# Optimization experiments

Measured on AMD Instinct MI355X. Metric: run time of the kernel, lower is better.

## Reference

```python
import jax, jax.numpy as jnp
import numpy as np

HIDDEN = 2048
N_HEADS = 32
N_KV_HEADS = 8
HEAD_DIM = HIDDEN // N_HEADS  # 64
ROPE_BASE = 10000.0
B, S = 2, 2048
NEG_INF = -1e9


def rotate_half(x):
    x1, x2 = jnp.split(x, 2, axis=-1)
    return jnp.concatenate((-x2, x1), axis=-1)


def rope_cos_sin(seq_len, head_dim, base, dtype):
    inv_freq = 1.0 / (base ** (jnp.arange(0, head_dim, 2, dtype=jnp.float32) / head_dim))
    pos = jnp.arange(seq_len, dtype=jnp.float32)
    freqs = jnp.outer(pos, inv_freq)              # [S, D/2]
    emb = jnp.concatenate((freqs, freqs), axis=-1)  # [S, D]
    return jnp.cos(emb).astype(dtype)[None, None], jnp.sin(emb).astype(dtype)[None, None]


def setup_inputs() -> dict:
    key = jax.random.key(0)
    ks = jax.random.split(key, 5)
    hidden_states = jax.random.normal(ks[0], (B, S, HIDDEN), dtype=jnp.float32)
    # causal additive mask, Llama-style
    causal = jnp.tril(jnp.ones((S, S), dtype=bool))
    attention_mask = jnp.where(causal, 0.0, NEG_INF).astype(jnp.float32)
    attention_mask = jnp.broadcast_to(attention_mask[None, None], (B, 1, S, S))
    sc = 1.0 / np.sqrt(HIDDEN)
    Wq = jax.random.normal(ks[1], (HIDDEN, HIDDEN), dtype=jnp.float32) * sc
    Wk = jax.random.normal(ks[2], (N_KV_HEADS * HEAD_DIM, HIDDEN), dtype=jnp.float32) * sc
    Wv = jax.random.normal(ks[3], (N_KV_HEADS * HEAD_DIM, HIDDEN), dtype=jnp.float32) * sc
    Wo = jax.random.normal(ks[4], (HIDDEN, HIDDEN), dtype=jnp.float32) * sc
    return {"hidden_states": hidden_states, "attention_mask": attention_mask,
            "Wq": Wq, "Wk": Wk, "Wv": Wv, "Wo": Wo}


def reference(hidden_states, attention_mask, Wq, Wk, Wv, Wo):
    b, s, _ = hidden_states.shape
    groups = N_HEADS // N_KV_HEADS
    # projections (torch Linear: x @ W.T)
    q = (hidden_states @ Wq.T).reshape(b, s, N_HEADS, HEAD_DIM).transpose(0, 2, 1, 3)      # [b,H,s,d]
    k = (hidden_states @ Wk.T).reshape(b, s, N_KV_HEADS, HEAD_DIM).transpose(0, 2, 1, 3)   # [b,Hk,s,d]
    v = (hidden_states @ Wv.T).reshape(b, s, N_KV_HEADS, HEAD_DIM).transpose(0, 2, 1, 3)
    cos, sin = rope_cos_sin(s, HEAD_DIM, ROPE_BASE, hidden_states.dtype)
    q = q * cos + rotate_half(q) * sin
    k = k * cos + rotate_half(k) * sin
    # GQA without materializing repeated K/V: view q as [b, Hk, g, s, d]
    qg = q.reshape(b, N_KV_HEADS, groups, s, HEAD_DIM)
    scores = jnp.einsum('bhgqd,bhkd->bhgqk', qg, k) / np.sqrt(HEAD_DIM)  # [b,Hk,g,s,s]
    scores = scores + attention_mask[:, :, None]                          # mask [b,1,1,s,s]
    probs = jax.nn.softmax(scores.astype(jnp.float32), axis=-1).astype(q.dtype)
    attn = jnp.einsum('bhgqk,bhkd->bhgqd', probs, v)                      # [b,Hk,g,s,d]
    attn = attn.reshape(b, N_HEADS, s, HEAD_DIM).transpose(0, 2, 1, 3).reshape(b, s, HIDDEN)
    return attn @ Wo.T
```

## Files before the change

kernel.cpp:

```cpp
#include <hip/hip_runtime.h>
#include <math.h>

#define HID 2048
#define NH 32
#define NKV 8
#define HD 64
#define BB 2
#define SS 2048
#define MTOT (BB * SS)

typedef __bf16 bf16;
typedef __bf16 bf16x8 __attribute__((ext_vector_type(8)));
typedef __bf16 bf16x4 __attribute__((ext_vector_type(4)));
typedef float f32x4 __attribute__((ext_vector_type(4)));

#define MFMA16(a, b, c) __builtin_amdgcn_mfma_f32_16x16x32_bf16((a), (b), (c), 0, 0, 0)

__device__ __forceinline__ void load_lds16(const void* g, void* l) {
  __builtin_amdgcn_global_load_lds((const __attribute__((address_space(1))) void*)g,
                                   (__attribute__((address_space(3))) void*)l, 16, 0, 0);
}

#define FENCE() asm volatile("" ::: "memory")
#define SYNC_VM(N) do { FENCE(); \
  asm volatile("s_waitcnt vmcnt(" #N ") lgkmcnt(0)" ::: "memory"); \
  __builtin_amdgcn_s_barrier(); FENCE(); } while (0)

__global__ void cvt_all(const float* __restrict__ hs, const float* __restrict__ Wq,
                        const float* __restrict__ Wk, const float* __restrict__ Wv,
                        const float* __restrict__ Wo,
                        bf16* __restrict__ A_b, bf16* __restrict__ Wq_b,
                        bf16* __restrict__ Wk_b, bf16* __restrict__ Wv_b,
                        bf16* __restrict__ Wo_b) {
  int bid = blockIdx.x;
  const float* src;
  bf16* dst;
  if (bid < 8192)       { src = hs; dst = A_b; }
  else if (bid < 12288) { src = Wq; dst = Wq_b; bid -= 8192; }
  else if (bid < 13312) { src = Wk; dst = Wk_b; bid -= 12288; }
  else if (bid < 14336) { src = Wv; dst = Wv_b; bid -= 13312; }
  else                  { src = Wo; dst = Wo_b; bid -= 14336; }
  int i = (bid * 256 + threadIdx.x) * 4;
  float4 v = *(const float4*)(src + i);
  bf16x4 o;
  o[0] = (bf16)v.x; o[1] = (bf16)v.y; o[2] = (bf16)v.z; o[3] = (bf16)v.w;
  *(bf16x4*)(dst + i) = o;
}

__device__ __forceinline__ void gemm_core_k64(const char* Agc, const char* Bgc,
                                              char* lds, f32x4 (&acc)[4][4]) {
  constexpr int ABYTES = 32768;
  constexpr int BUFB = 49152;
  constexpr int NT = HID / 64;

  const int tid = threadIdx.x;
  const int w = tid >> 6, lane = tid & 63;
  const int l16 = lane & 15, quad = lane >> 4;
  const int wr = w >> 1, wc = w & 1;
  const int wb = w * 1024;

  const int cu = (lane & 7) ^ ((lane >> 3) & 7);
  const char* gA = Agc + (size_t)(w * 8 + (lane >> 3)) * 4096 + cu * 16;
  const char* gB = Bgc + (size_t)(w * 8 + (lane >> 3)) * 4096 + cu * 16;

  const int aswz = l16 & 7;
  const int a_k0 = ((0 + quad) ^ aswz) * 16;
  const int a_k1 = ((4 + quad) ^ aswz) * 16;
  const int arow = (wr * 64 + l16) * 128;
  const int brow = (wc * 64 + l16) * 128;

#pragma unroll
  for (int t0 = 0; t0 < 2; ++t0) {
    char* lb = lds + t0 * BUFB;
#pragma unroll
    for (int j = 0; j < 4; ++j)
      load_lds16(gA + (size_t)j * (64 * 4096) + t0 * 128, lb + wb + j * 8192);
#pragma unroll
    for (int j = 0; j < 2; ++j)
      load_lds16(gB + (size_t)j * (64 * 4096) + t0 * 128, lb + ABYTES + wb + j * 8192);
  }

  char* cur = lds;
  char* stg = lds + 2 * BUFB;
  for (int kt = 0; kt < NT; ++kt) {
    SYNC_VM(6);
    const int ks = (kt + 2 < NT) ? (kt + 2) : (NT - 1);
    const size_t ko = (size_t)ks * 128;

#pragma unroll
    for (int j = 0; j < 4; ++j)
      load_lds16(gA + (size_t)j * (64 * 4096) + ko, stg + wb + j * 8192);
#pragma unroll
    for (int j = 0; j < 2; ++j)
      load_lds16(gB + (size_t)j * (64 * 4096) + ko, stg + ABYTES + wb + j * 8192);
    FENCE();

    const char* Ac = cur;
    const char* Bc = cur + ABYTES;
    bf16x8 af0[4], af1[4], bf0[4], bf1[4];
#pragma unroll
    for (int ni = 0; ni < 4; ++ni) {
      bf0[ni] = *(const bf16x8*)(Bc + brow + ni * 2048 + a_k0);
      bf1[ni] = *(const bf16x8*)(Bc + brow + ni * 2048 + a_k1);
    }
#pragma unroll
    for (int mi = 0; mi < 4; ++mi) {
      af0[mi] = *(const bf16x8*)(Ac + arow + mi * 2048 + a_k0);
      af1[mi] = *(const bf16x8*)(Ac + arow + mi * 2048 + a_k1);
    }
    __builtin_amdgcn_s_setprio(1);
#pragma unroll
    for (int mi = 0; mi < 4; ++mi)
#pragma unroll
      for (int ni = 0; ni < 4; ++ni) {
        acc[mi][ni] = MFMA16(af0[mi], bf0[ni], acc[mi][ni]);
        acc[mi][ni] = MFMA16(af1[mi], bf1[ni], acc[mi][ni]);
      }
    __builtin_amdgcn_s_setprio(0);

    cur = (cur == lds + 2 * BUFB) ? lds : cur + BUFB;
    stg = (stg == lds + 2 * BUFB) ? lds : stg + BUFB;
  }
  asm volatile("s_waitcnt vmcnt(0)" ::: "memory");
}

#define QSCALE 0.1803368801f
#define L2B 0.4152410118f
__global__ __launch_bounds__(512, 2) void gemm_qkv(const bf16* __restrict__ A,
                                                   const bf16* __restrict__ Wq,
                                                   const bf16* __restrict__ Wk,
                                                   const bf16* __restrict__ Wv,
                                                   bf16* __restrict__ Qb,
                                                   bf16* __restrict__ Kb,
                                                   bf16* __restrict__ Vt) {
  __shared__ __align__(16) char lds[3 * 49152];
  const int tileM = blockIdx.x * 256;
  const int n0 = blockIdx.y * 128;
  const bf16* Wp;
  int mode;
  if (n0 < HID) { Wp = Wq + (size_t)n0 * HID; mode = 0; }
  else if (n0 < HID + 512) { Wp = Wk + (size_t)(n0 - HID) * HID; mode = 1; }
  else { Wp = Wv + (size_t)(n0 - HID - 512) * HID; mode = 2; }

  f32x4 acc[4][4];
#pragma unroll
  for (int i = 0; i < 4; ++i)
#pragma unroll
    for (int j = 0; j < 4; ++j) acc[i][j] = (f32x4){0.f, 0.f, 0.f, 0.f};

  gemm_core_k64((const char*)(A + (size_t)tileM * HID), (const char*)Wp, lds, acc);

  const int tid = threadIdx.x;
  const int w = tid >> 6, lane = tid & 63;
  const int l16 = lane & 15, quad = lane >> 4;
  const int wr = w >> 1, wc = w & 1;
  const int mbase = tileM + wr * 64;
  const int cb = n0 + wc * 64;

  if (mode == 2) {
#pragma unroll
    for (int mi = 0; mi < 4; ++mi)
#pragma unroll
      for (int ni = 0; ni < 4; ++ni)
#pragma unroll
        for (int r = 0; r < 4; ++r) {
          int grow = mbase + mi * 16 + quad * 4 + r;
          int b = grow >> 11, spos = grow & (SS - 1);
          int nv = cb + ni * 16 + l16 - (HID + 512);
          Vt[(((size_t)(b * NKV + (nv >> 6))) * HD + (nv & 63)) * SS + spos] =
              (bf16)acc[mi][ni][r];
        }
  } else {
    const float inv0 = __builtin_amdgcn_exp2f(-(float)l16 * L2B);
    const float inv1 = __builtin_amdgcn_exp2f(-(float)(l16 + 16) * L2B);
#pragma unroll
    for (int mi = 0; mi < 4; ++mi) {
#pragma unroll
      for (int r = 0; r < 4; ++r) {
        int grow = mbase + mi * 16 + quad * 4 + r;
        int b = grow >> 11, spos = grow & (SS - 1);
        float sn0, cs0, sn1, cs1;
        sincosf((float)spos * inv0, &sn0, &cs0);
        sincosf((float)spos * inv1, &sn1, &cs1);
        float a0 = acc[mi][0][r], a1 = acc[mi][1][r];
        float a2 = acc[mi][2][r], a3 = acc[mi][3][r];
        float o0 = a0 * cs0 - a2 * sn0;
        float o2 = a2 * cs0 + a0 * sn0;
        float o1 = a1 * cs1 - a3 * sn1;
        float o3 = a3 * cs1 + a1 * sn1;
        if (mode == 0) {
          bf16* qp = Qb + (size_t)grow * HID + cb + l16;
          qp[0]  = (bf16)(o0 * QSCALE);
          qp[16] = (bf16)(o1 * QSCALE);
          qp[32] = (bf16)(o2 * QSCALE);
          qp[48] = (bf16)(o3 * QSCALE);
        } else {
          int kvh = (cb - HID) >> 6;
          bf16* kp = Kb + ((size_t)(b * NKV + kvh) * SS + spos) * HD + l16;
          kp[0]  = (bf16)o0;
          kp[16] = (bf16)o1;
          kp[32] = (bf16)o2;
          kp[48] = (bf16)o3;
        }
      }
    }
  }
}

__global__ __launch_bounds__(512, 2) void gemm_out(const bf16* __restrict__ A,
                                                   const bf16* __restrict__ Wo,
                                                   float* __restrict__ out) {
  __shared__ __align__(16) char lds[3 * 49152];
  const int tileM = blockIdx.x * 256;
  const int n0 = blockIdx.y * 128;
  f32x4 acc[4][4];
#pragma unroll
  for (int i = 0; i < 4; ++i)
#pragma unroll
    for (int j = 0; j < 4; ++j) acc[i][j] = (f32x4){0.f, 0.f, 0.f, 0.f};

  gemm_core_k64((const char*)(A + (size_t)tileM * HID),
                (const char*)(Wo + (size_t)n0 * HID), lds, acc);

  const int tid = threadIdx.x;
  const int w = tid >> 6, lane = tid & 63;
  const int l16 = lane & 15, quad = lane >> 4;
  const int wr = w >> 1, wc = w & 1;
#pragma unroll
  for (int mi = 0; mi < 4; ++mi)
#pragma unroll
    for (int ni = 0; ni < 4; ++ni)
#pragma unroll
      for (int r = 0; r < 4; ++r) {
        int grow = tileM + wr * 64 + mi * 16 + quad * 4 + r;
        int gcol = n0 + wc * 64 + ni * 16 + l16;
        out[(size_t)grow * HID + gcol] = acc[mi][ni][r];
      }
}

#define PSTR 72
__global__ __launch_bounds__(256, 3) void attn(const bf16* __restrict__ Qb,
                                               const bf16* __restrict__ Kb,
                                               const bf16* __restrict__ Vt,
                                               bf16* __restrict__ Ctx) {
  __shared__ bf16 Ktile[2][64 * 64];
  __shared__ bf16 Vtile[2][64 * 64];
  __shared__ bf16 Pbuf[4][32 * PSTR];
  const int tid = threadIdx.x;
  const int w = tid >> 6, lane = tid & 63;
  const int l16 = lane & 15, quad = lane >> 4;
  const int bh = blockIdx.y, b = bh >> 5, h = bh & 31, kvh = h >> 2;
  bf16* Pw = &Pbuf[w][0];
  const char* Kslice = (const char*)(Kb + ((size_t)(b * NKV + kvh)) * SS * HD);
  const char* Vslice = (const char*)(Vt + ((size_t)(b * NKV + kvh)) * HD * SS);
  const int qrel = w * 16 + l16;

  const int srow = (lane >> 3) & 7;
  const int pchunk = ((lane & 7) ^ srow) << 4;
  const int so = ((quad ^ (l16 & 7)) << 4);
  const int so2 = so ^ 64;

  const int xA = (int)blockIdx.x;

  int cur = 0;
  {
#pragma unroll
    for (int i = 0; i < 2; ++i) {
      const int r = w * 16 + i * 8 + srow;
      load_lds16(Kslice + (size_t)r * 128 + pchunk,
                 (char*)Ktile[0] + (w * 16 + i * 8) * 128);
      load_lds16(Vslice + (size_t)r * 4096 + pchunk,
                 (char*)Vtile[0] + (w * 16 + i * 8) * 128);
    }
  }

  for (int t = 0; t < 2; ++t) {
    const int X = t ? (15 - xA) : xA;
    const int qA = X * 128 + qrel;
    const int ktmax = 2 * X + 1;

    const bf16* QpA = Qb + ((size_t)(b * SS + qA)) * HID + h * HD + quad * 8;
    bf16x8 qa0 = *(const bf16x8*)QpA;
    bf16x8 qa1 = *(const bf16x8*)(QpA + 32);
    const bf16* QpB = QpA + (size_t)64 * HID;
    bf16x8 qbB0 = *(const bf16x8*)QpB;
    bf16x8 qbB1 = *(const bf16x8*)(QpB + 32);

    float lA = 0.f, lB = 0.f;
    f32x4 oA[4], oB[4];
#pragma unroll
    for (int d = 0; d < 4; ++d) {
      oA[d] = (f32x4){0.f, 0.f, 0.f, 0.f};
      oB[d] = (f32x4){0.f, 0.f, 0.f, 0.f};
    }

    for (int kt = 0; kt <= ktmax; ++kt) {
      __syncthreads();

      const bool have_next = (kt < ktmax) || (t == 0);
      if (have_next) {
        const int nkb = (kt < ktmax) ? (kt + 1) * 64 : 0;
        const int nb = cur ^ 1;
#pragma unroll
        for (int i = 0; i < 2; ++i) {
          const int r = w * 16 + i * 8 + srow;
          load_lds16(Kslice + (size_t)(nkb + r) * 128 + pchunk,
                     (char*)Ktile[nb] + (w * 16 + i * 8) * 128);
          load_lds16(Vslice + (size_t)r * 4096 + (size_t)nkb * 2 + pchunk,
                     (char*)Vtile[nb] + (w * 16 + i * 8) * 128);
        }
      }

      const char* Kc = (const char*)Ktile[cur] + l16 * 128;
      const char* Vc = (const char*)Vtile[cur] + l16 * 128;
      const bool skipA = (kt == ktmax);
      const bool diagA = (kt == ktmax - 1);
      const bool diagB = (kt == ktmax);

#pragma unroll
      for (int nt = 0; nt < 4; ++nt) {
        bf16x8 kf0 = *(const bf16x8*)(Kc + nt * 2048 + so);
        bf16x8 kf1 = *(const bf16x8*)(Kc + nt * 2048 + so2);
        const int krel = nt * 16 + quad * 4;

        bf16x4 pkA;
        if (skipA) {
          pkA[0] = (bf16)0.f; pkA[1] = (bf16)0.f;
          pkA[2] = (bf16)0.f; pkA[3] = (bf16)0.f;
        } else {
          f32x4 s = {0.f, 0.f, 0.f, 0.f};
          s = MFMA16(kf0, qa0, s);
          s = MFMA16(kf1, qa1, s);
          if (diagA) {
#pragma unroll
            for (int r = 0; r < 4; ++r) {
              float p = (krel + r > qrel) ? 0.f : __builtin_amdgcn_exp2f(s[r]);
              lA += p;
              pkA[r] = (bf16)p;
            }
          } else {
#pragma unroll
            for (int r = 0; r < 4; ++r) {
              float p = __builtin_amdgcn_exp2f(s[r]);
              lA += p;
              pkA[r] = (bf16)p;
            }
          }
        }
        *(bf16x4*)&Pw[l16 * PSTR + krel] = pkA;

        f32x4 sB = {0.f, 0.f, 0.f, 0.f};
        sB = MFMA16(kf0, qbB0, sB);
        sB = MFMA16(kf1, qbB1, sB);
        bf16x4 pkB;
        if (diagB) {
#pragma unroll
          for (int r = 0; r < 4; ++r) {
            float p = (krel + r > qrel) ? 0.f : __builtin_amdgcn_exp2f(sB[r]);
            lB += p;
            pkB[r] = (bf16)p;
          }
        } else {
#pragma unroll
          for (int r = 0; r < 4; ++r) {
            float p = __builtin_amdgcn_exp2f(sB[r]);
            lB += p;
            pkB[r] = (bf16)p;
          }
        }
        *(bf16x4*)&Pw[(16 + l16) * PSTR + krel] = pkB;
      }

      bf16x8 pA0 = *(const bf16x8*)&Pw[l16 * PSTR + quad * 8];
      bf16x8 pA1 = *(const bf16x8*)&Pw[l16 * PSTR + 32 + quad * 8];
      bf16x8 pB0 = *(const bf16x8*)&Pw[(16 + l16) * PSTR + quad * 8];
      bf16x8 pB1 = *(const bf16x8*)&Pw[(16 + l16) * PSTR + 32 + quad * 8];
#pragma unroll
      for (int dn = 0; dn < 4; ++dn) {
        bf16x8 v0 = *(const bf16x8*)(Vc + dn * 2048 + so);
        bf16x8 v1 = *(const bf16x8*)(Vc + dn * 2048 + so2);
        oA[dn] = MFMA16(v0, pA0, oA[dn]);
        oA[dn] = MFMA16(v1, pA1, oA[dn]);
        oB[dn] = MFMA16(v0, pB0, oB[dn]);
        oB[dn] = MFMA16(v1, pB1, oB[dn]);
      }
      cur ^= 1;
    }

    lA += __shfl_xor(lA, 16);
    lA += __shfl_xor(lA, 32);
    lB += __shfl_xor(lB, 16);
    lB += __shfl_xor(lB, 32);
    const float invA = 1.0f / lA;
    const float invB = 1.0f / lB;
    bf16* CpA = Ctx + ((size_t)(b * SS + qA)) * HID + h * HD + quad * 4;
    bf16* CpB = CpA + (size_t)64 * HID;
#pragma unroll
    for (int dn = 0; dn < 4; ++dn) {
      bf16x4 ovA, ovB;
#pragma unroll
      for (int r = 0; r < 4; ++r) {
        ovA[r] = (bf16)(oA[dn][r] * invA);
        ovB[r] = (bf16)(oB[dn][r] * invB);
      }
      *(bf16x4*)(CpA + dn * 16) = ovA;
      *(bf16x4*)(CpB + dn * 16) = ovB;
    }
  }
}

extern "C" void kernel_launch(void* const* d_in, const int* in_sizes, int n_in,
                              void* d_out, int out_size, void* d_ws, size_t ws_size,
                              hipStream_t stream) {
  const float* hs = (const float*)d_in[0];
  const float* Wq = (const float*)d_in[2];
  const float* Wk = (const float*)d_in[3];
  const float* Wv = (const float*)d_in[4];
  const float* Wo = (const float*)d_in[5];

  char* ws = (char*)d_ws;
  bf16* A_b  = (bf16*)(ws);
  bf16* Wq_b = (bf16*)(ws + 16777216);
  bf16* Wk_b = (bf16*)(ws + 25165824);
  bf16* Wv_b = (bf16*)(ws + 27262976);
  bf16* Wo_b = (bf16*)(ws + 29360128);
  bf16* Qb   = (bf16*)(ws + 37748736);
  bf16* Kb   = (bf16*)(ws + 54525952);
  bf16* Vt   = (bf16*)(ws + 58720256);
  bf16* Ctx  = A_b;

  cvt_all<<<18432, 256, 0, stream>>>(hs, Wq, Wk, Wv, Wo, A_b, Wq_b, Wk_b, Wv_b, Wo_b);
  gemm_qkv<<<dim3(MTOT / 256, 24), 512, 0, stream>>>(A_b, Wq_b, Wk_b, Wv_b, Qb, Kb, Vt);
  attn<<<dim3(8, BB * NH), 256, 0, stream>>>(Qb, Kb, Vt, Ctx);
  gemm_out<<<dim3(MTOT / 256, HID / 128), 512, 0, stream>>>(Ctx, Wo_b, (float*)d_out);
}
```

Baseline: 296.7 us.

## Use K=32 triple-buffered GEMM core for QKV and split out-proj loads into halves

The QKV projection switches to a new GEMM core with K-step 32, half the LDS footprint (3x24KB) and a new swizzled layout, and its launch bounds are raised to 4 blocks per CU. The goal is more resident blocks to hide memory latency. The output projection keeps K=64 but splits each step into two halves with an extra barrier, so the B-tile prefetch is issued after the first half of the MFMAs. The cost is more loop iterations and barriers per K, plus possible register pressure at the higher occupancy target.

```diff
diff --git a/kernel.cpp b/kernel.cpp
--- a/kernel.cpp
+++ b/kernel.cpp
@@ -47,8 +47,70 @@
   *(bf16x4*)(dst + i) = o;
 }
 
-__device__ __forceinline__ void gemm_core_k64(const char* Agc, const char* Bgc,
-                                              char* lds, f32x4 (&acc)[4][4]) {
+__device__ __forceinline__ void gemm_core256x128(const char* Agc, const char* Bgc,
+                                                 char* lds, f32x4 (&acc)[4][4]) {
+  constexpr int ABYTES = 16384;
+  constexpr int BUFB = 24576;
+  constexpr int NT = HID / 32;
+
+  const int tid = threadIdx.x;
+  const int w = tid >> 6, lane = tid & 63;
+  const int l16 = lane & 15, quad = lane >> 4;
+  const int wr = w >> 1, wc = w & 1;
+  const int wb = w * 1024;
+
+  const int cu = (tid & 7) ^ ((tid >> 3) & 7);
+  const int srcR0 = 2 * (tid >> 3) + (cu >> 2);
+  const int srcC = (cu & 3) * 16;
+  const char* gA = Agc + (size_t)srcR0 * (HID * 2) + srcC;
+  const char* gB = Bgc + (size_t)srcR0 * (HID * 2) + srcC;
+
+  const int acg16 = ((((l16 & 1) << 2) | quad) ^ ((l16 >> 1) & 7)) * 16;
+  const int aoff = (wr * 32 + (l16 >> 1)) * 128 + acg16;
+  const int boff = ABYTES + (wc * 32 + (l16 >> 1)) * 128 + acg16;
+
+#pragma unroll
+  for (int t0 = 0; t0 < 2; ++t0) {
+    char* lb = lds + t0 * BUFB;
+    load_lds16(gA + t0 * 64, lb + wb);
+    load_lds16(gA + (size_t)128 * (HID * 2) + t0 * 64, lb + 8192 + wb);
+    load_lds16(gB + t0 * 64, lb + ABYTES + wb);
+  }
+
+  char* cur = lds;
+  char* stg = lds + 2 * BUFB;
+  for (int kt = 0; kt < NT; ++kt) {
+    SYNC_VM(3);
+    const int ks = (kt + 2 < NT) ? (kt + 2) * 64 : (NT - 1) * 64;
+
+    load_lds16(gA + ks, stg + wb);
+    load_lds16(gA + (size_t)128 * (HID * 2) + ks, stg + 8192 + wb);
+    load_lds16(gB + ks, stg + ABYTES + wb);
+    FENCE();
+
+    bf16x8 af[4], bfr[4];
+#pragma unroll
+    for (int ni = 0; ni < 4; ++ni)
+      bfr[ni] = *(const bf16x8*)(cur + boff + ni * 1024);
+#pragma unroll
+    for (int mi = 0; mi < 4; ++mi)
+      af[mi] = *(const bf16x8*)(cur + aoff + mi * 1024);
+    __builtin_amdgcn_s_setprio(1);
+#pragma unroll
+    for (int mi = 0; mi < 4; ++mi)
+#pragma unroll
+      for (int ni = 0; ni < 4; ++ni)
+        acc[mi][ni] = MFMA16(af[mi], bfr[ni], acc[mi][ni]);
+    __builtin_amdgcn_s_setprio(0);
+
+    cur = (cur == lds + 2 * BUFB) ? lds : cur + BUFB;
+    stg = (stg == lds + 2 * BUFB) ? lds : stg + BUFB;
+  }
+  asm volatile("s_waitcnt vmcnt(0)" ::: "memory");
+}
+
+__device__ __forceinline__ void gemm_core_k64p(const char* Agc, const char* Bgc,
+                                               char* lds, f32x4 (&acc)[4][4]) {
   constexpr int ABYTES = 32768;
   constexpr int BUFB = 49152;
   constexpr int NT = HID / 64;
@@ -86,36 +148,48 @@
     SYNC_VM(6);
     const int ks = (kt + 2 < NT) ? (kt + 2) : (NT - 1);
     const size_t ko = (size_t)ks * 128;
+    const char* Ac = cur;
+    const char* Bc = cur + ABYTES;
 
 #pragma unroll
     for (int j = 0; j < 4; ++j)
       load_lds16(gA + (size_t)j * (64 * 4096) + ko, stg + wb + j * 8192);
+    FENCE();
+    bf16x8 af0[4], bf0[4];
+#pragma unroll
+    for (int ni = 0; ni < 4; ++ni)
+      bf0[ni] = *(const bf16x8*)(Bc + brow + ni * 2048 + a_k0);
+#pragma unroll
+    for (int mi = 0; mi < 4; ++mi)
+      af0[mi] = *(const bf16x8*)(Ac + arow + mi * 2048 + a_k0);
+    __builtin_amdgcn_s_setprio(1);
+#pragma unroll
+    for (int mi = 0; mi < 4; ++mi)
+#pragma unroll
+      for (int ni = 0; ni < 4; ++ni)
+        acc[mi][ni] = MFMA16(af0[mi], bf0[ni], acc[mi][ni]);
+    __builtin_amdgcn_s_setprio(0);
+    FENCE();
+    __builtin_amdgcn_s_barrier();
+    FENCE();
+
 #pragma unroll
     for (int j = 0; j < 2; ++j)
       load_lds16(gB + (size_t)j * (64 * 4096) + ko, stg + ABYTES + wb + j * 8192);
     FENCE();
-
-    const char* Ac = cur;
-    const char* Bc = cur + ABYTES;
-    bf16x8 af0[4], af1[4], bf0[4], bf1[4];
-#pragma unroll
-    for (int ni = 0; ni < 4; ++ni) {
-      bf0[ni] = *(const bf16x8*)(Bc + brow + ni * 2048 + a_k0);
+    bf16x8 af1[4], bf1[4];
+#pragma unroll
+    for (int ni = 0; ni < 4; ++ni)
       bf1[ni] = *(const bf16x8*)(Bc + brow + ni * 2048 + a_k1);
-    }
-#pragma unroll
-    for (int mi = 0; mi < 4; ++mi) {
-      af0[mi] = *(const bf16x8*)(Ac + arow + mi * 2048 + a_k0);
+#pragma unroll
+    for (int mi = 0; mi < 4; ++mi)
       af1[mi] = *(const bf16x8*)(Ac + arow + mi * 2048 + a_k1);
-    }
     __builtin_amdgcn_s_setprio(1);
 #pragma unroll
     for (int mi = 0; mi < 4; ++mi)
 #pragma unroll
-      for (int ni = 0; ni < 4; ++ni) {
-        acc[mi][ni] = MFMA16(af0[mi], bf0[ni], acc[mi][ni]);
+      for (int ni = 0; ni < 4; ++ni)
         acc[mi][ni] = MFMA16(af1[mi], bf1[ni], acc[mi][ni]);
-      }
     __builtin_amdgcn_s_setprio(0);
 
     cur = (cur == lds + 2 * BUFB) ? lds : cur + BUFB;
@@ -126,14 +200,14 @@
 
 #define QSCALE 0.1803368801f
 #define L2B 0.4152410118f
-__global__ __launch_bounds__(512, 2) void gemm_qkv(const bf16* __restrict__ A,
+__global__ __launch_bounds__(512, 4) void gemm_qkv(const bf16* __restrict__ A,
                                                    const bf16* __restrict__ Wq,
                                                    const bf16* __restrict__ Wk,
                                                    const bf16* __restrict__ Wv,
                                                    bf16* __restrict__ Qb,
                                                    bf16* __restrict__ Kb,
                                                    bf16* __restrict__ Vt) {
-  __shared__ __align__(16) char lds[3 * 49152];
+  __shared__ __align__(16) char lds[3 * 24576];
   const int tileM = blockIdx.x * 256;
   const int n0 = blockIdx.y * 128;
   const bf16* Wp;
@@ -148,7 +222,7 @@
 #pragma unroll
     for (int j = 0; j < 4; ++j) acc[i][j] = (f32x4){0.f, 0.f, 0.f, 0.f};
 
-  gemm_core_k64((const char*)(A + (size_t)tileM * HID), (const char*)Wp, lds, acc);
+  gemm_core256x128((const char*)(A + (size_t)tileM * HID), (const char*)Wp, lds, acc);
 
   const int tid = threadIdx.x;
   const int w = tid >> 6, lane = tid & 63;
@@ -219,8 +293,8 @@
 #pragma unroll
     for (int j = 0; j < 4; ++j) acc[i][j] = (f32x4){0.f, 0.f, 0.f, 0.f};
 
-  gemm_core_k64((const char*)(A + (size_t)tileM * HID),
-                (const char*)(Wo + (size_t)n0 * HID), lds, acc);
+  gemm_core_k64p((const char*)(A + (size_t)tileM * HID),
+                 (const char*)(Wo + (size_t)n0 * HID), lds, acc);
 
   const int tid = threadIdx.x;
   const int w = tid >> 6, lane = tid & 63;
```

Result: no change. 298.0 us (+0.4%).
